# Optimization experiments

Hardware: AMD Instinct MI355X
Metric: run time of the kernel (lower is better)

Reference implementation:

```python
import jax, jax.numpy as jnp
import numpy as np

NUM_NODES = 10000
NUM_EDGES = 640000
IN_FEAT = 128
OUT_FEAT = 128


def setup_inputs() -> dict:
    key = jax.random.key(0)
    k_x, k_e, k_w = jax.random.split(key, 3)
    x = jax.random.normal(k_x, (NUM_NODES, IN_FEAT), dtype=jnp.float32)
    edge_index = jax.random.randint(k_e, (2, NUM_EDGES), 0, NUM_NODES, dtype=jnp.int64)
    # Xavier-uniform W, zeros B (as in the torch init)
    limit = float(np.sqrt(6.0 / (IN_FEAT + OUT_FEAT)))
    W = jax.random.uniform(k_w, (OUT_FEAT, IN_FEAT), dtype=jnp.float32, minval=-limit, maxval=limit)
    B = jnp.zeros((OUT_FEAT, IN_FEAT), dtype=jnp.float32)
    return {"x": x, "edge_index": edge_index, "W": W, "B": B}


def reference(x, edge_index, W, B):
    num_nodes = x.shape[0]
    src, dst = edge_index[0], edge_index[1]
    # gather messages from source nodes, scatter-add into destination nodes
    messages = x[src]  # [num_edges, in_feat]
    agg = jax.ops.segment_sum(messages, dst, num_segments=num_nodes)  # [num_nodes, in_feat]
    # in-degree normalization (zero-degree nodes -> divide by 1)
    deg = jax.ops.segment_sum(jnp.ones_like(dst, dtype=x.dtype), dst, num_segments=num_nodes)
    deg = jnp.where(deg == 0, jnp.asarray(1.0, x.dtype), deg)
    agg = agg / deg[:, None]
    # dual linear combine: messages @ W.T + x @ B.T
    return agg @ W.T + x @ B.T
```

## Files before the change

kernel.cpp:

```cpp
#include <hip/hip_runtime.h>

#define NUM_NODES 10000
#define NUM_EDGES 640000
#define FEAT 128
#define K2 256
#define NPB 32
#define NBUCK 313
#define BCAP 2560
#define DEG_MAX 128
#define ASTRIDE 136

using bf16x8 = __attribute__((ext_vector_type(8))) short;
using f32x4 = __attribute__((ext_vector_type(4))) float;

static __device__ inline unsigned short f2bf(float f) {
  union { float f; unsigned int u; } v;
  v.f = f;
  unsigned int r = v.u + 0x7FFF + ((v.u >> 16) & 1);
  return (unsigned short)(r >> 16);
}
static __device__ inline float bf2f(unsigned short u) {
  union { unsigned int u; float f; } v;
  v.u = ((unsigned int)u) << 16;
  return v.f;
}

__global__ __launch_bounds__(256) void convert_bin_kernel(
    const float* __restrict__ x,
    const float* __restrict__ W,
    const float* __restrict__ B,
    const int* __restrict__ src,
    const int* __restrict__ dst,
    unsigned short* __restrict__ Xbf,
    unsigned short* __restrict__ Bbuf,
    unsigned int* __restrict__ staging,
    int* __restrict__ bucket_cnt) {
  __shared__ int hist[NBUCK];
  __shared__ int wbase[NBUCK];
  int blk = blockIdx.x;
  int tid = threadIdx.x;
  if (blk < 1250) {
    int base = (blk * 256 + tid) * 4;
    float4 v = *(const float4*)(x + base);
    ushort4 o;
    o.x = f2bf(v.x); o.y = f2bf(v.y); o.z = f2bf(v.z); o.w = f2bf(v.w);
    *(ushort4*)(Xbf + base) = o;
  } else if (blk < 1282) {
    int base = ((blk - 1250) * 256 + tid) * 4;
    const float* srcp;
    size_t dstoff;
    if (base < FEAT * FEAT) {
      int o = base >> 7, k = base & 127;
      srcp = W + base;
      dstoff = (size_t)o * K2 + k;
    } else {
      int b = base - FEAT * FEAT;
      int o = b >> 7, k = b & 127;
      srcp = B + b;
      dstoff = (size_t)o * K2 + FEAT + k;
    }
    float4 v = *(const float4*)srcp;
    ushort4 ov;
    ov.x = f2bf(v.x); ov.y = f2bf(v.y); ov.z = f2bf(v.z); ov.w = f2bf(v.w);
    *(ushort4*)(Bbuf + dstoff) = ov;
  } else {
    int ebase = (blk - 1282) * 4096;
    for (int t = tid; t < NBUCK; t += 256) hist[t] = 0;
    __syncthreads();
    int s[16], d[16];
#pragma unroll
    for (int i = 0; i < 16; ++i) {
      int e = ebase + tid + i * 256;
      if (e < NUM_EDGES) {
        s[i] = src[e];
        d[i] = dst[e];
        atomicAdd(&hist[d[i] >> 5], 1);
      } else {
        s[i] = -1;
        d[i] = 0;
      }
    }
    __syncthreads();
    for (int t = tid; t < NBUCK; t += 256) {
      wbase[t] = atomicAdd(&bucket_cnt[t], hist[t]);
      hist[t] = 0;
    }
    __syncthreads();
#pragma unroll
    for (int i = 0; i < 16; ++i) {
      if (s[i] >= 0) {
        int bkt = d[i] >> 5;
        int r = atomicAdd(&hist[bkt], 1);
        int off = wbase[bkt] + r;
        if (off < BCAP)
          staging[(size_t)bkt * BCAP + off] =
              ((unsigned int)(d[i] & 31) << 16) | (unsigned int)s[i];
      }
    }
  }
}

__global__ __launch_bounds__(512) void agg_gemm_kernel(
    const unsigned int* __restrict__ staging,
    const int* __restrict__ bucket_cnt,
    const unsigned short* __restrict__ Xbf,
    const unsigned short* __restrict__ Bbuf,
    float* __restrict__ out) {
  __shared__ unsigned short lcsr[NPB * DEG_MAX];
  __shared__ int lcnt[NPB];
  __shared__ __attribute__((aligned(16))) unsigned short aggA[NPB * ASTRIDE];
  int b = blockIdx.x;
  int tid = threadIdx.x;
  if (tid < NPB) lcnt[tid] = 0;
  __syncthreads();
  int nb = bucket_cnt[b];
  if (nb > BCAP) nb = BCAP;
  const unsigned int* st = staging + (size_t)b * BCAP;
  for (int i = tid; i < nb; i += 512) {
    unsigned int e = st[i];
    int dl = e >> 16;
    int pos = atomicAdd(&lcnt[dl], 1);
    if (pos < DEG_MAX) lcsr[dl * DEG_MAX + pos] = (unsigned short)(e & 0xFFFF);
  }
  __syncthreads();

  int grp = tid >> 5;
  int lane = tid & 31;
#pragma unroll
  for (int it = 0; it < 2; ++it) {
    int nl = it * 16 + grp;
    int deg = (b * NPB + nl < NUM_NODES) ? lcnt[nl] : 0;
    if (deg > DEG_MAX) deg = DEG_MAX;
    const unsigned short* row = lcsr + nl * DEG_MAX;
    float a0[4] = {0.f, 0.f, 0.f, 0.f};
    float a1[4] = {0.f, 0.f, 0.f, 0.f};
    float a2[4] = {0.f, 0.f, 0.f, 0.f};
    float a3[4] = {0.f, 0.f, 0.f, 0.f};
    int e = 0;
    for (; e + 4 <= deg; e += 4) {
      int s0 = row[e], s1 = row[e + 1], s2 = row[e + 2], s3 = row[e + 3];
      ushort4 v0 = *(const ushort4*)(Xbf + (size_t)s0 * FEAT + lane * 4);
      ushort4 v1 = *(const ushort4*)(Xbf + (size_t)s1 * FEAT + lane * 4);
      ushort4 v2 = *(const ushort4*)(Xbf + (size_t)s2 * FEAT + lane * 4);
      ushort4 v3 = *(const ushort4*)(Xbf + (size_t)s3 * FEAT + lane * 4);
      a0[0] += bf2f(v0.x); a0[1] += bf2f(v0.y); a0[2] += bf2f(v0.z); a0[3] += bf2f(v0.w);
      a1[0] += bf2f(v1.x); a1[1] += bf2f(v1.y); a1[2] += bf2f(v1.z); a1[3] += bf2f(v1.w);
      a2[0] += bf2f(v2.x); a2[1] += bf2f(v2.y); a2[2] += bf2f(v2.z); a2[3] += bf2f(v2.w);
      a3[0] += bf2f(v3.x); a3[1] += bf2f(v3.y); a3[2] += bf2f(v3.z); a3[3] += bf2f(v3.w);
    }
    for (; e < deg; ++e) {
      int s0 = row[e];
      ushort4 v0 = *(const ushort4*)(Xbf + (size_t)s0 * FEAT + lane * 4);
      a0[0] += bf2f(v0.x); a0[1] += bf2f(v0.y); a0[2] += bf2f(v0.z); a0[3] += bf2f(v0.w);
    }
    float sc = (deg == 0) ? 1.0f : (1.0f / (float)deg);
    ushort4 o;
    o.x = f2bf((a0[0] + a1[0] + a2[0] + a3[0]) * sc);
    o.y = f2bf((a0[1] + a1[1] + a2[1] + a3[1]) * sc);
    o.z = f2bf((a0[2] + a1[2] + a2[2] + a3[2]) * sc);
    o.w = f2bf((a0[3] + a1[3] + a2[3] + a3[3]) * sc);
    *(ushort4*)(aggA + nl * ASTRIDE + lane * 4) = o;
  }
  __syncthreads();

  int w = tid >> 6;
  int l = tid & 63;
  int r = l & 15;
  int g = l >> 4;
  int rt = w >> 2;
  int ct0 = w & 3;
  int arl = rt * 16 + r;
  int arg = b * NPB + arl;
  if (arg >= NUM_NODES) arg = NUM_NODES - 1;

  f32x4 acc0 = {}, acc1 = {};
#pragma unroll
  for (int ks = 0; ks < 8; ++ks) {
    bf16x8 a;
    if (ks < 4)
      a = *(const bf16x8*)(aggA + arl * ASTRIDE + ks * 32 + g * 8);
    else
      a = *(const bf16x8*)(Xbf + (size_t)arg * FEAT + (ks - 4) * 32 + g * 8);
    int kb = ks * 32 + g * 8;
    bf16x8 b0 = *(const bf16x8*)(Bbuf + (size_t)(ct0 * 16 + r) * K2 + kb);
    bf16x8 b1 = *(const bf16x8*)(Bbuf + (size_t)((ct0 + 4) * 16 + r) * K2 + kb);
    acc0 = __builtin_amdgcn_mfma_f32_16x16x32_bf16(a, b0, acc0, 0, 0, 0);
    acc1 = __builtin_amdgcn_mfma_f32_16x16x32_bf16(a, b1, acc1, 0, 0, 0);
  }

#pragma unroll
  for (int j = 0; j < 4; ++j) {
    int rr = b * NPB + rt * 16 + g * 4 + j;
    if (rr < NUM_NODES) {
      out[(size_t)rr * FEAT + ct0 * 16 + r] = acc0[j];
      out[(size_t)rr * FEAT + (ct0 + 4) * 16 + r] = acc1[j];
    }
  }
}

extern "C" void kernel_launch(void* const* d_in, const int* in_sizes, int n_in,
                              void* d_out, int out_size, void* d_ws, size_t ws_size,
                              hipStream_t stream) {
  const float* x = (const float*)d_in[0];
  const int* ei = (const int*)d_in[1];
  const float* W = (const float*)d_in[2];
  const float* B = (const float*)d_in[3];
  float* out = (float*)d_out;

  unsigned short* Xbf = (unsigned short*)d_ws;
  unsigned short* Bbuf = Xbf + (size_t)NUM_NODES * FEAT;
  unsigned int* staging = (unsigned int*)(Bbuf + (size_t)FEAT * K2);
  int* bucket_cnt = (int*)(staging + (size_t)NBUCK * BCAP);

  const int* src = ei;
  const int* dst = ei + NUM_EDGES;

  hipMemsetAsync(bucket_cnt, 0, NBUCK * sizeof(int), stream);

  convert_bin_kernel<<<1439, 256, 0, stream>>>(x, W, B, src, dst, Xbf, Bbuf,
                                               staging, bucket_cnt);
  agg_gemm_kernel<<<NBUCK, 512, 0, stream>>>(staging, bucket_cnt, Xbf, Bbuf,
                                             out);
}
```

Baseline: 111.7 us.

## Replace global bucket atomics with per-block staging slots and widen aggregation block

The binning phase no longer reserves space with global atomicAdd on per-bucket counters. Each edge block writes into its own fixed-capacity slot per bucket and records a per-block count matrix, which also removes the memset. Binning blocks are scheduled first, and the aggregation kernel uses 1024 threads so each group handles one node and each wave one output tile. The intent is to cut global atomic contention and raise parallelism. The cost is a larger sparse staging scan, where each bucket reads 157x40 slots. Slots that exceed capacity 40 silently drop edges.

```diff
diff --git a/kernel.cpp b/kernel.cpp
--- a/kernel.cpp
+++ b/kernel.cpp
@@ -6,7 +6,9 @@
 #define K2 256
 #define NPB 32
 #define NBUCK 313
-#define BCAP 2560
+#define NBIN 157
+#define EPB 4096
+#define SCAP 40
 #define DEG_MAX 128
 #define ASTRIDE 136
 
@@ -34,19 +36,48 @@
     unsigned short* __restrict__ Xbf,
     unsigned short* __restrict__ Bbuf,
     unsigned int* __restrict__ staging,
-    int* __restrict__ bucket_cnt) {
+    int* __restrict__ cntmat) {
   __shared__ int hist[NBUCK];
-  __shared__ int wbase[NBUCK];
   int blk = blockIdx.x;
   int tid = threadIdx.x;
-  if (blk < 1250) {
-    int base = (blk * 256 + tid) * 4;
+  if (blk < NBIN) {
+    int ebase = blk * EPB;
+    for (int t = tid; t < NBUCK; t += 256) hist[t] = 0;
+    __syncthreads();
+    int s[16], d[16];
+#pragma unroll
+    for (int i = 0; i < 16; ++i) {
+      int e = ebase + tid + i * 256;
+      if (e < NUM_EDGES) {
+        s[i] = src[e];
+        d[i] = dst[e];
+      } else {
+        s[i] = -1;
+        d[i] = 0;
+      }
+    }
+    __syncthreads();
+#pragma unroll
+    for (int i = 0; i < 16; ++i) {
+      if (s[i] >= 0) {
+        int bkt = d[i] >> 5;
+        int r = atomicAdd(&hist[bkt], 1);
+        if (r < SCAP)
+          staging[((size_t)bkt * NBIN + blk) * SCAP + r] =
+              ((unsigned int)(d[i] & 31) << 16) | (unsigned int)s[i];
+      }
+    }
+    __syncthreads();
+    for (int t = tid; t < NBUCK; t += 256)
+      cntmat[(size_t)blk * NBUCK + t] = hist[t];
+  } else if (blk < 157 + 1250) {
+    int base = ((blk - NBIN) * 256 + tid) * 4;
     float4 v = *(const float4*)(x + base);
     ushort4 o;
     o.x = f2bf(v.x); o.y = f2bf(v.y); o.z = f2bf(v.z); o.w = f2bf(v.w);
     *(ushort4*)(Xbf + base) = o;
-  } else if (blk < 1282) {
-    int base = ((blk - 1250) * 256 + tid) * 4;
+  } else {
+    int base = ((blk - 1407) * 256 + tid) * 4;
     const float* srcp;
     size_t dstoff;
     if (base < FEAT * FEAT) {
@@ -63,75 +94,47 @@
     ushort4 ov;
     ov.x = f2bf(v.x); ov.y = f2bf(v.y); ov.z = f2bf(v.z); ov.w = f2bf(v.w);
     *(ushort4*)(Bbuf + dstoff) = ov;
-  } else {
-    int ebase = (blk - 1282) * 4096;
-    for (int t = tid; t < NBUCK; t += 256) hist[t] = 0;
-    __syncthreads();
-    int s[16], d[16];
-#pragma unroll
-    for (int i = 0; i < 16; ++i) {
-      int e = ebase + tid + i * 256;
-      if (e < NUM_EDGES) {
-        s[i] = src[e];
-        d[i] = dst[e];
-        atomicAdd(&hist[d[i] >> 5], 1);
-      } else {
-        s[i] = -1;
-        d[i] = 0;
-      }
-    }
-    __syncthreads();
-    for (int t = tid; t < NBUCK; t += 256) {
-      wbase[t] = atomicAdd(&bucket_cnt[t], hist[t]);
-      hist[t] = 0;
-    }
-    __syncthreads();
-#pragma unroll
-    for (int i = 0; i < 16; ++i) {
-      if (s[i] >= 0) {
-        int bkt = d[i] >> 5;
-        int r = atomicAdd(&hist[bkt], 1);
-        int off = wbase[bkt] + r;
-        if (off < BCAP)
-          staging[(size_t)bkt * BCAP + off] =
-              ((unsigned int)(d[i] & 31) << 16) | (unsigned int)s[i];
-      }
-    }
-  }
-}
-
-__global__ __launch_bounds__(512) void agg_gemm_kernel(
+  }
+}
+
+__global__ __launch_bounds__(1024) void agg_gemm_kernel(
     const unsigned int* __restrict__ staging,
-    const int* __restrict__ bucket_cnt,
+    const int* __restrict__ cntmat,
     const unsigned short* __restrict__ Xbf,
     const unsigned short* __restrict__ Bbuf,
     float* __restrict__ out) {
   __shared__ unsigned short lcsr[NPB * DEG_MAX];
   __shared__ int lcnt[NPB];
+  __shared__ int scnt[NBIN];
   __shared__ __attribute__((aligned(16))) unsigned short aggA[NPB * ASTRIDE];
   int b = blockIdx.x;
   int tid = threadIdx.x;
   if (tid < NPB) lcnt[tid] = 0;
+  for (int t = tid; t < NBIN; t += 1024) {
+    int c = cntmat[(size_t)t * NBUCK + b];
+    scnt[t] = (c > SCAP) ? SCAP : c;
+  }
   __syncthreads();
-  int nb = bucket_cnt[b];
-  if (nb > BCAP) nb = BCAP;
-  const unsigned int* st = staging + (size_t)b * BCAP;
-  for (int i = tid; i < nb; i += 512) {
-    unsigned int e = st[i];
-    int dl = e >> 16;
-    int pos = atomicAdd(&lcnt[dl], 1);
-    if (pos < DEG_MAX) lcsr[dl * DEG_MAX + pos] = (unsigned short)(e & 0xFFFF);
+  const unsigned int* stb = staging + (size_t)b * (NBIN * SCAP);
+  for (int i = tid; i < NBIN * SCAP; i += 1024) {
+    int blk = i / SCAP;
+    int slot = i - blk * SCAP;
+    if (slot < scnt[blk]) {
+      unsigned int e = stb[i];
+      int dl = e >> 16;
+      int pos = atomicAdd(&lcnt[dl], 1);
+      if (pos < DEG_MAX)
+        lcsr[dl * DEG_MAX + pos] = (unsigned short)(e & 0xFFFF);
+    }
   }
   __syncthreads();
 
   int grp = tid >> 5;
   int lane = tid & 31;
-#pragma unroll
-  for (int it = 0; it < 2; ++it) {
-    int nl = it * 16 + grp;
-    int deg = (b * NPB + nl < NUM_NODES) ? lcnt[nl] : 0;
+  {
+    int deg = (b * NPB + grp < NUM_NODES) ? lcnt[grp] : 0;
     if (deg > DEG_MAX) deg = DEG_MAX;
-    const unsigned short* row = lcsr + nl * DEG_MAX;
+    const unsigned short* row = lcsr + grp * DEG_MAX;
     float a0[4] = {0.f, 0.f, 0.f, 0.f};
     float a1[4] = {0.f, 0.f, 0.f, 0.f};
     float a2[4] = {0.f, 0.f, 0.f, 0.f};
@@ -159,7 +162,7 @@
     o.y = f2bf((a0[1] + a1[1] + a2[1] + a3[1]) * sc);
     o.z = f2bf((a0[2] + a1[2] + a2[2] + a3[2]) * sc);
     o.w = f2bf((a0[3] + a1[3] + a2[3] + a3[3]) * sc);
-    *(ushort4*)(aggA + nl * ASTRIDE + lane * 4) = o;
+    *(ushort4*)(aggA + grp * ASTRIDE + lane * 4) = o;
   }
   __syncthreads();
 
@@ -167,13 +170,13 @@
   int l = tid & 63;
   int r = l & 15;
   int g = l >> 4;
-  int rt = w >> 2;
-  int ct0 = w & 3;
+  int rt = w >> 3;
+  int ct = w & 7;
   int arl = rt * 16 + r;
   int arg = b * NPB + arl;
   if (arg >= NUM_NODES) arg = NUM_NODES - 1;
 
-  f32x4 acc0 = {}, acc1 = {};
+  f32x4 acc = {};
 #pragma unroll
   for (int ks = 0; ks < 8; ++ks) {
     bf16x8 a;
@@ -182,19 +185,14 @@
     else
       a = *(const bf16x8*)(Xbf + (size_t)arg * FEAT + (ks - 4) * 32 + g * 8);
     int kb = ks * 32 + g * 8;
-    bf16x8 b0 = *(const bf16x8*)(Bbuf + (size_t)(ct0 * 16 + r) * K2 + kb);
-    bf16x8 b1 = *(const bf16x8*)(Bbuf + (size_t)((ct0 + 4) * 16 + r) * K2 + kb);
-    acc0 = __builtin_amdgcn_mfma_f32_16x16x32_bf16(a, b0, acc0, 0, 0, 0);
-    acc1 = __builtin_amdgcn_mfma_f32_16x16x32_bf16(a, b1, acc1, 0, 0, 0);
+    bf16x8 bb = *(const bf16x8*)(Bbuf + (size_t)(ct * 16 + r) * K2 + kb);
+    acc = __builtin_amdgcn_mfma_f32_16x16x32_bf16(a, bb, acc, 0, 0, 0);
   }
 
 #pragma unroll
   for (int j = 0; j < 4; ++j) {
     int rr = b * NPB + rt * 16 + g * 4 + j;
-    if (rr < NUM_NODES) {
-      out[(size_t)rr * FEAT + ct0 * 16 + r] = acc0[j];
-      out[(size_t)rr * FEAT + (ct0 + 4) * 16 + r] = acc1[j];
-    }
+    if (rr < NUM_NODES) out[(size_t)rr * FEAT + ct * 16 + r] = acc[j];
   }
 }
 
@@ -210,15 +208,12 @@
   unsigned short* Xbf = (unsigned short*)d_ws;
   unsigned short* Bbuf = Xbf + (size_t)NUM_NODES * FEAT;
   unsigned int* staging = (unsigned int*)(Bbuf + (size_t)FEAT * K2);
-  int* bucket_cnt = (int*)(staging + (size_t)NBUCK * BCAP);
+  int* cntmat = (int*)(staging + (size_t)NBUCK * NBIN * SCAP);
 
   const int* src = ei;
   const int* dst = ei + NUM_EDGES;
 
-  hipMemsetAsync(bucket_cnt, 0, NBUCK * sizeof(int), stream);
-
   convert_bin_kernel<<<1439, 256, 0, stream>>>(x, W, B, src, dst, Xbf, Bbuf,
-                                               staging, bucket_cnt);
-  agg_gemm_kernel<<<NBUCK, 512, 0, stream>>>(staging, bucket_cnt, Xbf, Bbuf,
-                                             out);
-}
+                                               staging, cntmat);
+  agg_gemm_kernel<<<NBUCK, 1024, 0, stream>>>(staging, cntmat, Xbf, Bbuf, out);
+}
```

Result: faster. 104.8 us (-6.2%).
